# Optimization experiments

Measured on AMD Instinct MI355X. Metric: run time of the kernel, lower is better.

## Reference

```python
import jax, jax.numpy as jnp
import numpy as np

HIDDEN = 1024
NUM_EXPERTS = 64
MIN_K, MAX_K = 1, 4
THRESHOLD = 0.5
N_TOKENS = 32768


def setup_inputs() -> dict:
    key = jax.random.key(0)
    ks = jax.random.split(key, 6)
    std = 0.02
    h4 = HIDDEN // 4
    return {
        "hidden_states": jax.random.normal(ks[0], (N_TOKENS, HIDDEN), dtype=jnp.float32),
        "router_w": std * jax.random.normal(ks[1], (NUM_EXPERTS, HIDDEN), dtype=jnp.float32),
        "w1": std * jax.random.normal(ks[2], (h4, HIDDEN), dtype=jnp.float32),
        "b1": jnp.zeros((h4,), dtype=jnp.float32),
        "w2": std * jax.random.normal(ks[3], (1, h4), dtype=jnp.float32),
        "b2": jnp.zeros((1,), dtype=jnp.float32),
    }


def reference(hidden_states, router_w, w1, b1, w2, b2):
    # complexity predictor: Linear -> ReLU -> Linear -> Sigmoid, squeeze(-1)
    h = jax.nn.relu(hidden_states @ w1.T + b1)                     # [N, H/4]
    complexity = jax.nn.sigmoid(h @ w2.T + b2)[:, 0]               # [N]
    router_logits = hidden_states @ router_w.T                     # [N, E]

    adaptive_k = jnp.where(complexity > THRESHOLD, MAX_K, MIN_K)   # [N] int

    # vectorized adaptive top-k: take MAX_K everywhere, mask beyond k
    top_vals, top_idx = jax.lax.top_k(router_logits, MAX_K)        # [N, MAX_K]
    pos_mask = jnp.arange(MAX_K)[None, :] < adaptive_k[:, None]    # [N, MAX_K]
    masked_vals = jnp.where(pos_mask, top_vals, -jnp.inf)
    expert_weights = jax.nn.softmax(masked_vals, axis=-1)
    expert_weights = jnp.where(pos_mask, expert_weights, 0.0)      # zeros past k
    selected_experts = jnp.where(pos_mask, top_idx, 0)             # zeros past k

    # routing statistics
    probs = jax.nn.softmax(router_logits, axis=-1)                 # [N, E]
    expert_load = probs.mean(axis=0)                               # [E]
    load_variance = expert_load.var(ddof=1)                        # torch .var() is unbiased
    entropy = -(probs * jnp.log(probs + 1e-8)).sum(axis=-1).mean()

    return router_logits, selected_experts, expert_weights, load_variance, entropy
```

## Files before the change

### kernel.cpp

```cpp
#include <hip/hip_runtime.h>
#include <hip/hip_bf16.h>
#include <math.h>

#define NTOK 32768
#define HID  1024
#define NEXP 64
#define H4   256

typedef __attribute__((ext_vector_type(8))) short bf16x8;
typedef __attribute__((ext_vector_type(8))) unsigned short u16x8;
typedef __attribute__((ext_vector_type(4))) float f32x4;

static __device__ __forceinline__ ushort f2bf(float x) {
    unsigned u = __float_as_uint(x);
    unsigned r = (u + 0x7FFFu + ((u >> 16) & 1u)) >> 16;
    return (ushort)r;
}

static __device__ __forceinline__ void split3r(float x, ushort &h, ushort &m, ushort &l) {
    h = f2bf(x);
    const float r1 = x - __uint_as_float(((unsigned)h) << 16);
    m = f2bf(r1);
    const float r2 = r1 - __uint_as_float(((unsigned)m) << 16);
    l = f2bf(r2);
}

#define SWZ(row, us) ((us) ^ (((row) & 7) << 3))

__global__ __launch_bounds__(256) void prep_kernel(
    const float* __restrict__ W1, const float* __restrict__ RW,
    ushort* __restrict__ W1f, ushort* __restrict__ RWf)
{
    if (blockIdx.x < 256) {
        const int id = blockIdx.x * 256 + threadIdx.x;
        const int c  = id >> 8;
        const int k0 = (id & 255) * 4;
        const float4 v = *(const float4*)(W1 + (size_t)c * HID + k0);
        const int p = k0 >> 5, quad = (k0 >> 3) & 3, kk = k0 & 7;
        const int cg = c >> 6, j = (c >> 4) & 3, l15 = c & 15;
        const int lane = quad * 16 + l15;
        const size_t base = (size_t)p * 16384 + cg * 4096 + j * 1024 + lane * 8 + kk;
        const float xs[4] = {v.x, v.y, v.z, v.w};
        ushort hv[4], lv[4];
#pragma unroll
        for (int q = 0; q < 4; q++) {
            const ushort h = f2bf(xs[q]);
            hv[q] = h;
            lv[q] = f2bf(xs[q] - __uint_as_float(((unsigned)h) << 16));
        }
        *(ushort4*)(W1f + base)       = make_ushort4(hv[0], hv[1], hv[2], hv[3]);
        *(ushort4*)(W1f + base + 512) = make_ushort4(lv[0], lv[1], lv[2], lv[3]);
    } else {
        const int e  = blockIdx.x - 256;
        const int k0 = threadIdx.x * 4;
        const float4 v = *(const float4*)(RW + (size_t)e * HID + k0);
        const int p = k0 >> 5, quad = (k0 >> 3) & 3, kk = k0 & 7;
        const int cg = e >> 4, l15 = e & 15;
        const int lane = quad * 16 + l15;
        const size_t base = (size_t)p * 6144 + cg * 1536 + lane * 8 + kk;
        const float xs[4] = {v.x, v.y, v.z, v.w};
        ushort h[4], m[4], l[4];
#pragma unroll
        for (int q = 0; q < 4; q++) split3r(xs[q], h[q], m[q], l[q]);
        *(ushort4*)(RWf + base)        = make_ushort4(h[0], h[1], h[2], h[3]);
        *(ushort4*)(RWf + base + 512)  = make_ushort4(m[0], m[1], m[2], m[3]);
        *(ushort4*)(RWf + base + 1024) = make_ushort4(l[0], l[1], l[2], l[3]);
    }
}

template<int PH>
__device__ __forceinline__ void kstep(
    int p, int cg, int lane, int quad, int l15, int row, int kc,
    const float* __restrict__ xsrc,
    const ushort* __restrict__ RWf, const ushort* __restrict__ W1f,
    ushort (&Xh)[2][2048], ushort (&Xm)[2][2048], ushort (&Xl)[2][2048],
    bf16x8 (&rwh)[2], bf16x8 (&rwm)[2], bf16x8 (&rwl)[2],
    bf16x8 (&bwh)[2][4], bf16x8 (&bwl)[2][4],
    float4 (&xp)[2][2],
    f32x4 (&accL)[4], f32x4 (&accP)[4][4])
{
    {
        const ushort* __restrict__ rwp =
            RWf + (size_t)((p + 1) & 31) * 6144 + cg * 1536 + lane * 8;
        rwh[PH ^ 1] = *(const bf16x8*)(rwp);
        rwm[PH ^ 1] = *(const bf16x8*)(rwp + 512);
        rwl[PH ^ 1] = *(const bf16x8*)(rwp + 1024);
    }
    {
        const ushort* __restrict__ w1p =
            W1f + (size_t)((p + 1) & 31) * 16384 + cg * 4096 + lane * 8;
#pragma unroll
        for (int j = 0; j < 4; ++j) {
            bwh[PH ^ 1][j] = *(const bf16x8*)(w1p + j * 1024);
            bwl[PH ^ 1][j] = *(const bf16x8*)(w1p + j * 1024 + 512);
        }
    }
    xp[PH ^ 1][0] = *(const float4*)(xsrc + (size_t)((p + 2) & 31) * 32);
    xp[PH ^ 1][1] = *(const float4*)(xsrc + (size_t)((p + 2) & 31) * 32 + 4);

    bf16x8 axh[4], axm[4], axl[4];
#pragma unroll
    for (int f = 0; f < 4; ++f) {
        const int ra = f * 16 + l15;
        const int ua = SWZ(ra, ra * 32 + quad * 8);
        axh[f] = *(const bf16x8*)&Xh[PH][ua];
        axm[f] = *(const bf16x8*)&Xm[PH][ua];
        axl[f] = *(const bf16x8*)&Xl[PH][ua];
    }

    {
        const float xs[8] = {xp[PH][0].x, xp[PH][0].y, xp[PH][0].z, xp[PH][0].w,
                             xp[PH][1].x, xp[PH][1].y, xp[PH][1].z, xp[PH][1].w};
        u16x8 sh, sm, sl;
#pragma unroll
        for (int q = 0; q < 8; ++q) {
            ushort h, m, l;
            split3r(xs[q], h, m, l);
            sh[q] = h; sm[q] = m; sl[q] = l;
        }
        const int us = SWZ(row, row * 32 + kc * 8);
        *(u16x8*)&Xh[PH ^ 1][us] = sh;
        *(u16x8*)&Xm[PH ^ 1][us] = sm;
        *(u16x8*)&Xl[PH ^ 1][us] = sl;
    }

#pragma unroll
    for (int f = 0; f < 4; ++f) {
        accL[f] = __builtin_amdgcn_mfma_f32_16x16x32_bf16(axh[f], rwh[PH], accL[f], 0, 0, 0);
        accL[f] = __builtin_amdgcn_mfma_f32_16x16x32_bf16(axm[f], rwh[PH], accL[f], 0, 0, 0);
        accL[f] = __builtin_amdgcn_mfma_f32_16x16x32_bf16(axh[f], rwm[PH], accL[f], 0, 0, 0);
        accL[f] = __builtin_amdgcn_mfma_f32_16x16x32_bf16(axl[f], rwh[PH], accL[f], 0, 0, 0);
        accL[f] = __builtin_amdgcn_mfma_f32_16x16x32_bf16(axh[f], rwl[PH], accL[f], 0, 0, 0);
        accL[f] = __builtin_amdgcn_mfma_f32_16x16x32_bf16(axm[f], rwm[PH], accL[f], 0, 0, 0);
    }
#pragma unroll
    for (int j = 0; j < 4; ++j)
#pragma unroll
        for (int f = 0; f < 4; ++f) {
            accP[f][j] = __builtin_amdgcn_mfma_f32_16x16x32_bf16(axh[f], bwh[PH][j], accP[f][j], 0, 0, 0);
            accP[f][j] = __builtin_amdgcn_mfma_f32_16x16x32_bf16(axm[f], bwh[PH][j], accP[f][j], 0, 0, 0);
            accP[f][j] = __builtin_amdgcn_mfma_f32_16x16x32_bf16(axh[f], bwl[PH][j], accP[f][j], 0, 0, 0);
        }

    asm volatile("s_waitcnt lgkmcnt(0)" ::: "memory");
    __builtin_amdgcn_s_barrier();
    __builtin_amdgcn_sched_barrier(0);
}

__global__ __launch_bounds__(256, 2) void fused_mfma(
    const float* __restrict__ X,
    const ushort* __restrict__ RWf, const ushort* __restrict__ W1f,
    const float* __restrict__ B1, const float* __restrict__ W2,
    const float* __restrict__ B2,
    float* __restrict__ logits, float* __restrict__ sel,
    float* __restrict__ wts, float* __restrict__ load_sum,
    float* __restrict__ ent_sum)
{
    __shared__ __align__(16) ushort Xh[2][2048], Xm[2][2048], Xl[2][2048];
    __shared__ float red[4][64];
    __shared__ float Lt[64][65];

    const int tid  = threadIdx.x;
    const int lane = tid & 63;
    const int cg   = tid >> 6;
    const int quad = lane >> 4, l15 = lane & 15;
    const int tok0 = blockIdx.x * 64;

    const int row = tid >> 2;
    const int kc  = tid & 3;

    f32x4 accL[4];
    f32x4 accP[4][4];
#pragma unroll
    for (int f = 0; f < 4; f++) {
        accL[f] = (f32x4){0.f, 0.f, 0.f, 0.f};
#pragma unroll
        for (int j = 0; j < 4; j++) accP[f][j] = (f32x4){0.f, 0.f, 0.f, 0.f};
    }

    const float* __restrict__ xsrc = X + (size_t)(tok0 + row) * HID + kc * 8;

    bf16x8 rwh[2], rwm[2], rwl[2];
    bf16x8 bwh[2][4], bwl[2][4];
    float4 xp[2][2];

    {
        const float4 a0 = *(const float4*)(xsrc);
        const float4 a1 = *(const float4*)(xsrc + 4);
        const float xs[8] = {a0.x, a0.y, a0.z, a0.w, a1.x, a1.y, a1.z, a1.w};
        u16x8 sh, sm, sl;
#pragma unroll
        for (int q = 0; q < 8; ++q) {
            ushort h, m, l;
            split3r(xs[q], h, m, l);
            sh[q] = h; sm[q] = m; sl[q] = l;
        }
        const int us = SWZ(row, row * 32 + kc * 8);
        *(u16x8*)&Xh[0][us] = sh;
        *(u16x8*)&Xm[0][us] = sm;
        *(u16x8*)&Xl[0][us] = sl;
    }
    {
        const ushort* __restrict__ rwp = RWf + (size_t)cg * 1536 + lane * 8;
        rwh[0] = *(const bf16x8*)(rwp);
        rwm[0] = *(const bf16x8*)(rwp + 512);
        rwl[0] = *(const bf16x8*)(rwp + 1024);
        const ushort* __restrict__ w1p = W1f + (size_t)cg * 4096 + lane * 8;
#pragma unroll
        for (int j = 0; j < 4; ++j) {
            bwh[0][j] = *(const bf16x8*)(w1p + j * 1024);
            bwl[0][j] = *(const bf16x8*)(w1p + j * 1024 + 512);
        }
    }
    xp[0][0] = *(const float4*)(xsrc + 32);
    xp[0][1] = *(const float4*)(xsrc + 36);
    __syncthreads();

    for (int p = 0; p < 32; p += 2) {
        kstep<0>(p,     cg, lane, quad, l15, row, kc, xsrc, RWf, W1f,
                 Xh, Xm, Xl, rwh, rwm, rwl, bwh, bwl, xp, accL, accP);
        kstep<1>(p + 1, cg, lane, quad, l15, row, kc, xsrc, RWf, W1f,
                 Xh, Xm, Xl, rwh, rwm, rwl, bwh, bwl, xp, accL, accP);
    }

#pragma unroll
    for (int f = 0; f < 4; ++f)
#pragma unroll
        for (int r = 0; r < 4; ++r) {
            const int trow = f * 16 + quad * 4 + r;
            logits[(size_t)(tok0 + trow) * NEXP + cg * 16 + l15] = accL[f][r];
            Lt[trow][cg * 16 + l15] = accL[f][r];
        }

    float w2r[4], b1r[4];
#pragma unroll
    for (int j = 0; j < 4; ++j) {
        const int col = (cg * 4 + j) * 16 + l15;
        w2r[j] = W2[col];
        b1r[j] = B1[col];
    }
#pragma unroll
    for (int f = 0; f < 4; ++f) {
#pragma unroll
        for (int r = 0; r < 4; ++r) {
            float s = 0.f;
#pragma unroll
            for (int j = 0; j < 4; ++j) {
                const float hval = accP[f][j][r] + b1r[j];
                s = fmaf(w2r[j], fmaxf(hval, 0.f), s);
            }
            s += __shfl_xor(s, 1);
            s += __shfl_xor(s, 2);
            s += __shfl_xor(s, 4);
            s += __shfl_xor(s, 8);
            if (l15 == 0)
                red[cg][f * 16 + quad * 4 + r] = s;
        }
    }
    __syncthreads();

    if (cg == 0) {
        const int tok = tok0 + lane;

        float r[64];
#pragma unroll
        for (int e = 0; e < 64; e++) r[e] = Lt[lane][e];

        float v0 = -1e30f, v1 = -1e30f, v2 = -1e30f, v3 = -1e30f;
        int   i0 = 0, i1 = 0, i2 = 0, i3 = 0;
#pragma unroll
        for (int e = 0; e < 64; e++) {
            const float v = r[e];
            if (v > v3) {
                if (v > v2) {
                    if (v > v1) {
                        if (v > v0) { v3=v2;i3=i2; v2=v1;i2=i1; v1=v0;i1=i0; v0=v;i0=e; }
                        else        { v3=v2;i3=i2; v2=v1;i2=i1; v1=v;i1=e; }
                    } else          { v3=v2;i3=i2; v2=v;i2=e; }
                } else              { v3=v;i3=e; }
            }
        }

        const float s2 = red[0][lane] + red[1][lane] + red[2][lane]
                       + red[3][lane] + B2[0];
        const bool k4 = (s2 > 0.f);

        float w0, w1v, w2v, w3v;
        int   s1i, s2i, s3i;
        if (k4) {
            const float e0 = expf(v0 - v0), e1 = expf(v1 - v0);
            const float e2 = expf(v2 - v0), e3 = expf(v3 - v0);
            const float inv4 = 1.f / (e0 + e1 + e2 + e3);
            w0 = e0 * inv4; w1v = e1 * inv4; w2v = e2 * inv4; w3v = e3 * inv4;
            s1i = i1; s2i = i2; s3i = i3;
        } else {
            w0 = 1.f; w1v = 0.f; w2v = 0.f; w3v = 0.f;
            s1i = 0; s2i = 0; s3i = 0;
        }
        {
            float4 sv = {(float)i0, (float)s1i, (float)s2i, (float)s3i};
            float4 wv = {w0, w1v, w2v, w3v};
            *(float4*)(sel + (size_t)tok * 4) = sv;
            *(float4*)(wts + (size_t)tok * 4) = wv;
        }

        const float mx = v0;
        float S = 0.f, pz = 0.f;
#pragma unroll
        for (int e = 0; e < 64; e++) {
            const float z = r[e] - mx;
            const float t = expf(z);
            S += t; pz = fmaf(t, z, pz);
            r[e] = t;
        }
        const float inv = 1.f / S;
        float ent = logf(S) - pz * inv;

        float myload = 0.f;
#pragma unroll
        for (int e = 0; e < 64; e++) {
            float s = r[e] * inv;
            s += __shfl_xor(s, 1);
            s += __shfl_xor(s, 2);
            s += __shfl_xor(s, 4);
            s += __shfl_xor(s, 8);
            s += __shfl_xor(s, 16);
            s += __shfl_xor(s, 32);
            if (lane == e) myload = s;
        }
        atomicAdd(&load_sum[lane], myload);

        ent += __shfl_xor(ent, 1);
        ent += __shfl_xor(ent, 2);
        ent += __shfl_xor(ent, 4);
        ent += __shfl_xor(ent, 8);
        ent += __shfl_xor(ent, 16);
        ent += __shfl_xor(ent, 32);
        if (lane == 0) atomicAdd(ent_sum, ent);
    }
}

__global__ void finalize_kernel(const float* __restrict__ load_sum,
                                const float* __restrict__ ent_sum,
                                float* __restrict__ out_scal)
{
    const int lane = threadIdx.x;
    const float le = load_sum[lane] * (1.f / (float)NTOK);
    float s = le;
#pragma unroll
    for (int o = 32; o >= 1; o >>= 1) s += __shfl_xor(s, o);
    const float mean = s * (1.f / 64.f);
    const float d = le - mean;
    float v = d * d;
#pragma unroll
    for (int o = 32; o >= 1; o >>= 1) v += __shfl_xor(v, o);
    if (lane == 0) {
        out_scal[0] = v * (1.f / 63.f);
        out_scal[1] = ent_sum[0] * (1.f / (float)NTOK);
    }
}

extern "C" void kernel_launch(void* const* d_in, const int* in_sizes, int n_in,
                              void* d_out, int out_size, void* d_ws, size_t ws_size,
                              hipStream_t stream) {
    const float* X  = (const float*)d_in[0];
    const float* RW = (const float*)d_in[1];
    const float* W1 = (const float*)d_in[2];
    const float* B1 = (const float*)d_in[3];
    const float* W2 = (const float*)d_in[4];
    const float* B2 = (const float*)d_in[5];

    float* out    = (float*)d_out;
    float* logits = out;
    float* sel    = out + (size_t)NTOK * NEXP;
    float* wts    = sel + (size_t)NTOK * 4;
    float* scal   = wts + (size_t)NTOK * 4;

    float* s2ws     = (float*)d_ws;
    float* load_sum = s2ws + NTOK;
    float* ent_sum  = load_sum + 64;
    ushort* W1f = (ushort*)(s2ws + NTOK + 256);
    ushort* RWf = W1f + (size_t)32 * 16384;

    hipMemsetAsync(load_sum, 0, 65 * sizeof(float), stream);

    prep_kernel<<<320, 256, 0, stream>>>(W1, RW, W1f, RWf);
    fused_mfma<<<NTOK / 64, 256, 0, stream>>>(X, RWf, W1f, B1, W2, B2,
                                              logits, sel, wts, load_sum, ent_sum);
    finalize_kernel<<<1, 64, 0, stream>>>(load_sum, ent_sum, scal);
}
```

Baseline: 254.7 us.

## Switch to 32x32x16 MFMA tiles with 2x2 wave layout

Result: slower. 285.8 us (+12.2%).

```diff
diff --git a/kernel.cpp b/kernel.cpp
--- a/kernel.cpp
+++ b/kernel.cpp
@@ -7,9 +7,9 @@
 #define NEXP 64
 #define H4   256
 
-typedef __attribute__((ext_vector_type(8))) short bf16x8;
-typedef __attribute__((ext_vector_type(8))) unsigned short u16x8;
-typedef __attribute__((ext_vector_type(4))) float f32x4;
+typedef __attribute__((ext_vector_type(8)))  short bf16x8;
+typedef __attribute__((ext_vector_type(8)))  unsigned short u16x8;
+typedef __attribute__((ext_vector_type(16))) float f32x16;
 
 static __device__ __forceinline__ ushort f2bf(float x) {
     unsigned u = __float_as_uint(x);
@@ -36,10 +36,13 @@
         const int c  = id >> 8;
         const int k0 = (id & 255) * 4;
         const float4 v = *(const float4*)(W1 + (size_t)c * HID + k0);
-        const int p = k0 >> 5, quad = (k0 >> 3) & 3, kk = k0 & 7;
-        const int cg = c >> 6, j = (c >> 4) & 3, l15 = c & 15;
-        const int lane = quad * 16 + l15;
-        const size_t base = (size_t)p * 16384 + cg * 4096 + j * 1024 + lane * 8 + kk;
+        const int p  = k0 >> 5;
+        const int ks = (k0 >> 4) & 1;
+        const int h5 = (k0 >> 3) & 1;
+        const int i0 = k0 & 7;
+        const int tcj = c >> 5, c31 = c & 31;
+        const int lane = h5 * 32 + c31;
+        const size_t base = (size_t)p * 16384 + tcj * 2048 + ks * 1024 + lane * 8 + i0;
         const float xs[4] = {v.x, v.y, v.z, v.w};
         ushort hv[4], lv[4];
 #pragma unroll
@@ -54,10 +57,13 @@
         const int e  = blockIdx.x - 256;
         const int k0 = threadIdx.x * 4;
         const float4 v = *(const float4*)(RW + (size_t)e * HID + k0);
-        const int p = k0 >> 5, quad = (k0 >> 3) & 3, kk = k0 & 7;
-        const int cg = e >> 4, l15 = e & 15;
-        const int lane = quad * 16 + l15;
-        const size_t base = (size_t)p * 6144 + cg * 1536 + lane * 8 + kk;
+        const int p  = k0 >> 5;
+        const int ks = (k0 >> 4) & 1;
+        const int h5 = (k0 >> 3) & 1;
+        const int i0 = k0 & 7;
+        const int tc = e >> 5, c31 = e & 31;
+        const int lane = h5 * 32 + c31;
+        const size_t base = (size_t)p * 6144 + tc * 3072 + ks * 1536 + lane * 8 + i0;
         const float xs[4] = {v.x, v.y, v.z, v.w};
         ushort h[4], m[4], l[4];
 #pragma unroll
@@ -70,42 +76,42 @@
 
 template<int PH>
 __device__ __forceinline__ void kstep(
-    int p, int cg, int lane, int quad, int l15, int row, int kc,
+    int p, int tr, int tc, int lane, int l31, int h5, int row, int kc,
     const float* __restrict__ xsrc,
     const ushort* __restrict__ RWf, const ushort* __restrict__ W1f,
     ushort (&Xh)[2][2048], ushort (&Xm)[2][2048], ushort (&Xl)[2][2048],
-    bf16x8 (&rwh)[2], bf16x8 (&rwm)[2], bf16x8 (&rwl)[2],
-    bf16x8 (&bwh)[2][4], bf16x8 (&bwl)[2][4],
     float4 (&xp)[2][2],
-    f32x4 (&accL)[4], f32x4 (&accP)[4][4])
+    f32x16 &accL, f32x16 (&accP)[4])
 {
-    {
-        const ushort* __restrict__ rwp =
-            RWf + (size_t)((p + 1) & 31) * 6144 + cg * 1536 + lane * 8;
-        rwh[PH ^ 1] = *(const bf16x8*)(rwp);
-        rwm[PH ^ 1] = *(const bf16x8*)(rwp + 512);
-        rwl[PH ^ 1] = *(const bf16x8*)(rwp + 1024);
-    }
-    {
-        const ushort* __restrict__ w1p =
-            W1f + (size_t)((p + 1) & 31) * 16384 + cg * 4096 + lane * 8;
+    const ushort* __restrict__ rwp = RWf + (size_t)p * 6144 + tc * 3072 + lane * 8;
+    bf16x8 rwh[2], rwm[2], rwl[2];
+#pragma unroll
+    for (int ks = 0; ks < 2; ++ks) {
+        rwh[ks] = *(const bf16x8*)(rwp + ks * 1536);
+        rwm[ks] = *(const bf16x8*)(rwp + ks * 1536 + 512);
+        rwl[ks] = *(const bf16x8*)(rwp + ks * 1536 + 1024);
+    }
+    const ushort* __restrict__ w1p = W1f + (size_t)p * 16384 + (tc * 4) * 2048 + lane * 8;
+    bf16x8 bwh[2][4], bwl[2][4];
+#pragma unroll
+    for (int ks = 0; ks < 2; ++ks)
 #pragma unroll
         for (int j = 0; j < 4; ++j) {
-            bwh[PH ^ 1][j] = *(const bf16x8*)(w1p + j * 1024);
-            bwl[PH ^ 1][j] = *(const bf16x8*)(w1p + j * 1024 + 512);
-        }
-    }
+            bwh[ks][j] = *(const bf16x8*)(w1p + j * 2048 + ks * 1024);
+            bwl[ks][j] = *(const bf16x8*)(w1p + j * 2048 + ks * 1024 + 512);
+        }
+
     xp[PH ^ 1][0] = *(const float4*)(xsrc + (size_t)((p + 2) & 31) * 32);
     xp[PH ^ 1][1] = *(const float4*)(xsrc + (size_t)((p + 2) & 31) * 32 + 4);
 
-    bf16x8 axh[4], axm[4], axl[4];
-#pragma unroll
-    for (int f = 0; f < 4; ++f) {
-        const int ra = f * 16 + l15;
-        const int ua = SWZ(ra, ra * 32 + quad * 8);
-        axh[f] = *(const bf16x8*)&Xh[PH][ua];
-        axm[f] = *(const bf16x8*)&Xm[PH][ua];
-        axl[f] = *(const bf16x8*)&Xl[PH][ua];
+    const int arow = tr * 32 + l31;
+    bf16x8 axh[2], axm[2], axl[2];
+#pragma unroll
+    for (int ks = 0; ks < 2; ++ks) {
+        const int ua = SWZ(arow, arow * 32 + ks * 16 + h5 * 8);
+        axh[ks] = *(const bf16x8*)&Xh[PH][ua];
+        axm[ks] = *(const bf16x8*)&Xm[PH][ua];
+        axl[ks] = *(const bf16x8*)&Xl[PH][ua];
     }
 
     {
@@ -125,22 +131,20 @@
     }
 
 #pragma unroll
-    for (int f = 0; f < 4; ++f) {
-        accL[f] = __builtin_amdgcn_mfma_f32_16x16x32_bf16(axh[f], rwh[PH], accL[f], 0, 0, 0);
-        accL[f] = __builtin_amdgcn_mfma_f32_16x16x32_bf16(axm[f], rwh[PH], accL[f], 0, 0, 0);
-        accL[f] = __builtin_amdgcn_mfma_f32_16x16x32_bf16(axh[f], rwm[PH], accL[f], 0, 0, 0);
-        accL[f] = __builtin_amdgcn_mfma_f32_16x16x32_bf16(axl[f], rwh[PH], accL[f], 0, 0, 0);
-        accL[f] = __builtin_amdgcn_mfma_f32_16x16x32_bf16(axh[f], rwl[PH], accL[f], 0, 0, 0);
-        accL[f] = __builtin_amdgcn_mfma_f32_16x16x32_bf16(axm[f], rwm[PH], accL[f], 0, 0, 0);
-    }
-#pragma unroll
-    for (int j = 0; j < 4; ++j)
-#pragma unroll
-        for (int f = 0; f < 4; ++f) {
-            accP[f][j] = __builtin_amdgcn_mfma_f32_16x16x32_bf16(axh[f], bwh[PH][j], accP[f][j], 0, 0, 0);
-            accP[f][j] = __builtin_amdgcn_mfma_f32_16x16x32_bf16(axm[f], bwh[PH][j], accP[f][j], 0, 0, 0);
-            accP[f][j] = __builtin_amdgcn_mfma_f32_16x16x32_bf16(axh[f], bwl[PH][j], accP[f][j], 0, 0, 0);
-        }
+    for (int ks = 0; ks < 2; ++ks) {
+        accL = __builtin_amdgcn_mfma_f32_32x32x16_bf16(axh[ks], rwh[ks], accL, 0, 0, 0);
+        accL = __builtin_amdgcn_mfma_f32_32x32x16_bf16(axm[ks], rwh[ks], accL, 0, 0, 0);
+        accL = __builtin_amdgcn_mfma_f32_32x32x16_bf16(axh[ks], rwm[ks], accL, 0, 0, 0);
+        accL = __builtin_amdgcn_mfma_f32_32x32x16_bf16(axl[ks], rwh[ks], accL, 0, 0, 0);
+        accL = __builtin_amdgcn_mfma_f32_32x32x16_bf16(axh[ks], rwl[ks], accL, 0, 0, 0);
+        accL = __builtin_amdgcn_mfma_f32_32x32x16_bf16(axm[ks], rwm[ks], accL, 0, 0, 0);
+#pragma unroll
+        for (int j = 0; j < 4; ++j) {
+            accP[j] = __builtin_amdgcn_mfma_f32_32x32x16_bf16(axh[ks], bwh[ks][j], accP[j], 0, 0, 0);
+            accP[j] = __builtin_amdgcn_mfma_f32_32x32x16_bf16(axm[ks], bwh[ks][j], accP[j], 0, 0, 0);
+            accP[j] = __builtin_amdgcn_mfma_f32_32x32x16_bf16(axh[ks], bwl[ks][j], accP[j], 0, 0, 0);
+        }
+    }
 
     asm volatile("s_waitcnt lgkmcnt(0)" ::: "memory");
     __builtin_amdgcn_s_barrier();
@@ -157,31 +161,32 @@
     float* __restrict__ ent_sum)
 {
     __shared__ __align__(16) ushort Xh[2][2048], Xm[2][2048], Xl[2][2048];
-    __shared__ float red[4][64];
+    __shared__ float red[2][64];
     __shared__ float Lt[64][65];
 
     const int tid  = threadIdx.x;
     const int lane = tid & 63;
-    const int cg   = tid >> 6;
-    const int quad = lane >> 4, l15 = lane & 15;
+    const int w    = tid >> 6;
+    const int tr   = w >> 1;
+    const int tc   = w & 1;
+    const int l31  = lane & 31;
+    const int h5   = lane >> 5;
     const int tok0 = blockIdx.x * 64;
 
     const int row = tid >> 2;
     const int kc  = tid & 3;
 
-    f32x4 accL[4];
-    f32x4 accP[4][4];
-#pragma unroll
-    for (int f = 0; f < 4; f++) {
-        accL[f] = (f32x4){0.f, 0.f, 0.f, 0.f};
-#pragma unroll
-        for (int j = 0; j < 4; j++) accP[f][j] = (f32x4){0.f, 0.f, 0.f, 0.f};
-    }
+    f32x16 accL;
+    f32x16 accP[4];
+#pragma unroll
+    for (int i = 0; i < 16; i++) accL[i] = 0.f;
+#pragma unroll
+    for (int j = 0; j < 4; j++)
+#pragma unroll
+        for (int i = 0; i < 16; i++) accP[j][i] = 0.f;
 
     const float* __restrict__ xsrc = X + (size_t)(tok0 + row) * HID + kc * 8;
 
-    bf16x8 rwh[2], rwm[2], rwl[2];
-    bf16x8 bwh[2][4], bwl[2][4];
     float4 xp[2][2];
 
     {
@@ -200,66 +205,51 @@
         *(u16x8*)&Xm[0][us] = sm;
         *(u16x8*)&Xl[0][us] = sl;
     }
-    {
-        const ushort* __restrict__ rwp = RWf + (size_t)cg * 1536 + lane * 8;
-        rwh[0] = *(const bf16x8*)(rwp);
-        rwm[0] = *(const bf16x8*)(rwp + 512);
-        rwl[0] = *(const bf16x8*)(rwp + 1024);
-        const ushort* __restrict__ w1p = W1f + (size_t)cg * 4096 + lane * 8;
-#pragma unroll
-        for (int j = 0; j < 4; ++j) {
-            bwh[0][j] = *(const bf16x8*)(w1p + j * 1024);
-            bwl[0][j] = *(const bf16x8*)(w1p + j * 1024 + 512);
-        }
-    }
     xp[0][0] = *(const float4*)(xsrc + 32);
     xp[0][1] = *(const float4*)(xsrc + 36);
     __syncthreads();
 
     for (int p = 0; p < 32; p += 2) {
-        kstep<0>(p,     cg, lane, quad, l15, row, kc, xsrc, RWf, W1f,
-                 Xh, Xm, Xl, rwh, rwm, rwl, bwh, bwl, xp, accL, accP);
-        kstep<1>(p + 1, cg, lane, quad, l15, row, kc, xsrc, RWf, W1f,
-                 Xh, Xm, Xl, rwh, rwm, rwl, bwh, bwl, xp, accL, accP);
-    }
-
-#pragma unroll
-    for (int f = 0; f < 4; ++f)
-#pragma unroll
-        for (int r = 0; r < 4; ++r) {
-            const int trow = f * 16 + quad * 4 + r;
-            logits[(size_t)(tok0 + trow) * NEXP + cg * 16 + l15] = accL[f][r];
-            Lt[trow][cg * 16 + l15] = accL[f][r];
-        }
+        kstep<0>(p,     tr, tc, lane, l31, h5, row, kc, xsrc, RWf, W1f,
+                 Xh, Xm, Xl, xp, accL, accP);
+        kstep<1>(p + 1, tr, tc, lane, l31, h5, row, kc, xsrc, RWf, W1f,
+                 Xh, Xm, Xl, xp, accL, accP);
+    }
+
+#pragma unroll
+    for (int r = 0; r < 16; ++r) {
+        const int orow = (r & 3) + 8 * (r >> 2) + 4 * h5;
+        const int trow = tr * 32 + orow;
+        logits[(size_t)(tok0 + trow) * NEXP + tc * 32 + l31] = accL[r];
+        Lt[trow][tc * 32 + l31] = accL[r];
+    }
 
     float w2r[4], b1r[4];
 #pragma unroll
     for (int j = 0; j < 4; ++j) {
-        const int col = (cg * 4 + j) * 16 + l15;
+        const int col = (tc * 4 + j) * 32 + l31;
         w2r[j] = W2[col];
         b1r[j] = B1[col];
     }
 #pragma unroll
-    for (int f = 0; f < 4; ++f) {
-#pragma unroll
-        for (int r = 0; r < 4; ++r) {
-            float s = 0.f;
-#pragma unroll
-            for (int j = 0; j < 4; ++j) {
-                const float hval = accP[f][j][r] + b1r[j];
-                s = fmaf(w2r[j], fmaxf(hval, 0.f), s);
-            }
-            s += __shfl_xor(s, 1);
-            s += __shfl_xor(s, 2);
-            s += __shfl_xor(s, 4);
-            s += __shfl_xor(s, 8);
-            if (l15 == 0)
-                red[cg][f * 16 + quad * 4 + r] = s;
-        }
+    for (int r = 0; r < 16; ++r) {
+        float s = 0.f;
+#pragma unroll
+        for (int j = 0; j < 4; ++j) {
+            const float hval = accP[j][r] + b1r[j];
+            s = fmaf(w2r[j], fmaxf(hval, 0.f), s);
+        }
+        s += __shfl_xor(s, 1);
+        s += __shfl_xor(s, 2);
+        s += __shfl_xor(s, 4);
+        s += __shfl_xor(s, 8);
+        s += __shfl_xor(s, 16);
+        if (l31 == 0)
+            red[tc][tr * 32 + (r & 3) + 8 * (r >> 2) + 4 * h5] = s;
     }
     __syncthreads();
 
-    if (cg == 0) {
+    if (w == 0) {
         const int tok = tok0 + lane;
 
         float r[64];
@@ -281,8 +271,7 @@
             }
         }
 
-        const float s2 = red[0][lane] + red[1][lane] + red[2][lane]
-                       + red[3][lane] + B2[0];
+        const float s2 = red[0][lane] + red[1][lane] + B2[0];
         const bool k4 = (s2 > 0.f);
 
         float w0, w1v, w2v, w3v;
```

## Load X fragments directly from global into registers, dropping LDS staging and barriers

Applied to the files above, without the earlier changes.

After: 327.5 us. 28.6% more time.

```diff
diff --git a/kernel.cpp b/kernel.cpp
--- a/kernel.cpp
+++ b/kernel.cpp
@@ -8,7 +8,6 @@
 #define H4   256
 
 typedef __attribute__((ext_vector_type(8))) short bf16x8;
-typedef __attribute__((ext_vector_type(8))) unsigned short u16x8;
 typedef __attribute__((ext_vector_type(4))) float f32x4;
 
 static __device__ __forceinline__ ushort f2bf(float x) {
@@ -24,8 +23,6 @@
     const float r2 = r1 - __uint_as_float(((unsigned)m) << 16);
     l = f2bf(r2);
 }
-
-#define SWZ(row, us) ((us) ^ (((row) & 7) << 3))
 
 __global__ __launch_bounds__(256) void prep_kernel(
     const float* __restrict__ W1, const float* __restrict__ RW,
@@ -70,15 +67,20 @@
 
 template<int PH>
 __device__ __forceinline__ void kstep(
-    int p, int cg, int lane, int quad, int l15, int row, int kc,
-    const float* __restrict__ xsrc,
+    int p, int cg, int lane, int quad, int l15,
+    const float* __restrict__ xrow0,
     const ushort* __restrict__ RWf, const ushort* __restrict__ W1f,
-    ushort (&Xh)[2][2048], ushort (&Xm)[2][2048], ushort (&Xl)[2][2048],
     bf16x8 (&rwh)[2], bf16x8 (&rwm)[2], bf16x8 (&rwl)[2],
-    bf16x8 (&bwh)[2][4], bf16x8 (&bwl)[2][4],
-    float4 (&xp)[2][2],
+    float4 (&xa)[2][4][2],
     f32x4 (&accL)[4], f32x4 (&accP)[4][4])
 {
+    const ushort* __restrict__ w1p = W1f + (size_t)p * 16384 + cg * 4096 + lane * 8;
+    bf16x8 bwh[4], bwl[4];
+#pragma unroll
+    for (int j = 0; j < 4; ++j) {
+        bwh[j] = *(const bf16x8*)(w1p + j * 1024);
+        bwl[j] = *(const bf16x8*)(w1p + j * 1024 + 512);
+    }
     {
         const ushort* __restrict__ rwp =
             RWf + (size_t)((p + 1) & 31) * 6144 + cg * 1536 + lane * 8;
@@ -87,64 +89,39 @@
         rwl[PH ^ 1] = *(const bf16x8*)(rwp + 1024);
     }
     {
-        const ushort* __restrict__ w1p =
-            W1f + (size_t)((p + 1) & 31) * 16384 + cg * 4096 + lane * 8;
+        const int kn = ((p + 1) & 31) * 32 + quad * 8;
+#pragma unroll
+        for (int f = 0; f < 4; ++f) {
+            const float* __restrict__ src = xrow0 + (size_t)(f * 16 + l15) * HID + kn;
+            xa[PH ^ 1][f][0] = *(const float4*)(src);
+            xa[PH ^ 1][f][1] = *(const float4*)(src + 4);
+        }
+    }
+
+#pragma unroll
+    for (int f = 0; f < 4; ++f) {
+        const float4 a0 = xa[PH][f][0], a1 = xa[PH][f][1];
+        const float xs[8] = {a0.x, a0.y, a0.z, a0.w, a1.x, a1.y, a1.z, a1.w};
+        ushort hv[8], mv[8], lv[8];
+#pragma unroll
+        for (int q = 0; q < 8; ++q) split3r(xs[q], hv[q], mv[q], lv[q]);
+        bf16x8 axh, axm, axl;
+#pragma unroll
+        for (int q = 0; q < 8; ++q) { axh[q] = (short)hv[q]; axm[q] = (short)mv[q]; axl[q] = (short)lv[q]; }
+
+        accL[f] = __builtin_amdgcn_mfma_f32_16x16x32_bf16(axh, rwh[PH], accL[f], 0, 0, 0);
+        accL[f] = __builtin_amdgcn_mfma_f32_16x16x32_bf16(axm, rwh[PH], accL[f], 0, 0, 0);
+        accL[f] = __builtin_amdgcn_mfma_f32_16x16x32_bf16(axh, rwm[PH], accL[f], 0, 0, 0);
+        accL[f] = __builtin_amdgcn_mfma_f32_16x16x32_bf16(axl, rwh[PH], accL[f], 0, 0, 0);
+        accL[f] = __builtin_amdgcn_mfma_f32_16x16x32_bf16(axh, rwl[PH], accL[f], 0, 0, 0);
+        accL[f] = __builtin_amdgcn_mfma_f32_16x16x32_bf16(axm, rwm[PH], accL[f], 0, 0, 0);
 #pragma unroll
         for (int j = 0; j < 4; ++j) {
-            bwh[PH ^ 1][j] = *(const bf16x8*)(w1p + j * 1024);
-            bwl[PH ^ 1][j] = *(const bf16x8*)(w1p + j * 1024 + 512);
-        }
-    }
-    xp[PH ^ 1][0] = *(const float4*)(xsrc + (size_t)((p + 2) & 31) * 32);
-    xp[PH ^ 1][1] = *(const float4*)(xsrc + (size_t)((p + 2) & 31) * 32 + 4);
-
-    bf16x8 axh[4], axm[4], axl[4];
-#pragma unroll
-    for (int f = 0; f < 4; ++f) {
-        const int ra = f * 16 + l15;
-        const int ua = SWZ(ra, ra * 32 + quad * 8);
-        axh[f] = *(const bf16x8*)&Xh[PH][ua];
-        axm[f] = *(const bf16x8*)&Xm[PH][ua];
-        axl[f] = *(const bf16x8*)&Xl[PH][ua];
-    }
-
-    {
-        const float xs[8] = {xp[PH][0].x, xp[PH][0].y, xp[PH][0].z, xp[PH][0].w,
-                             xp[PH][1].x, xp[PH][1].y, xp[PH][1].z, xp[PH][1].w};
-        u16x8 sh, sm, sl;
-#pragma unroll
-        for (int q = 0; q < 8; ++q) {
-            ushort h, m, l;
-            split3r(xs[q], h, m, l);
-            sh[q] = h; sm[q] = m; sl[q] = l;
-        }
-        const int us = SWZ(row, row * 32 + kc * 8);
-        *(u16x8*)&Xh[PH ^ 1][us] = sh;
-        *(u16x8*)&Xm[PH ^ 1][us] = sm;
-        *(u16x8*)&Xl[PH ^ 1][us] = sl;
-    }
-
-#pragma unroll
-    for (int f = 0; f < 4; ++f) {
-        accL[f] = __builtin_amdgcn_mfma_f32_16x16x32_bf16(axh[f], rwh[PH], accL[f], 0, 0, 0);
-        accL[f] = __builtin_amdgcn_mfma_f32_16x16x32_bf16(axm[f], rwh[PH], accL[f], 0, 0, 0);
-        accL[f] = __builtin_amdgcn_mfma_f32_16x16x32_bf16(axh[f], rwm[PH], accL[f], 0, 0, 0);
-        accL[f] = __builtin_amdgcn_mfma_f32_16x16x32_bf16(axl[f], rwh[PH], accL[f], 0, 0, 0);
-        accL[f] = __builtin_amdgcn_mfma_f32_16x16x32_bf16(axh[f], rwl[PH], accL[f], 0, 0, 0);
-        accL[f] = __builtin_amdgcn_mfma_f32_16x16x32_bf16(axm[f], rwm[PH], accL[f], 0, 0, 0);
-    }
-#pragma unroll
-    for (int j = 0; j < 4; ++j)
-#pragma unroll
-        for (int f = 0; f < 4; ++f) {
-            accP[f][j] = __builtin_amdgcn_mfma_f32_16x16x32_bf16(axh[f], bwh[PH][j], accP[f][j], 0, 0, 0);
-            accP[f][j] = __builtin_amdgcn_mfma_f32_16x16x32_bf16(axm[f], bwh[PH][j], accP[f][j], 0, 0, 0);
-            accP[f][j] = __builtin_amdgcn_mfma_f32_16x16x32_bf16(axh[f], bwl[PH][j], accP[f][j], 0, 0, 0);
-        }
-
-    asm volatile("s_waitcnt lgkmcnt(0)" ::: "memory");
-    __builtin_amdgcn_s_barrier();
-    __builtin_amdgcn_sched_barrier(0);
+            accP[f][j] = __builtin_amdgcn_mfma_f32_16x16x32_bf16(axh, bwh[j], accP[f][j], 0, 0, 0);
+            accP[f][j] = __builtin_amdgcn_mfma_f32_16x16x32_bf16(axm, bwh[j], accP[f][j], 0, 0, 0);
+            accP[f][j] = __builtin_amdgcn_mfma_f32_16x16x32_bf16(axh, bwl[j], accP[f][j], 0, 0, 0);
+        }
+    }
 }
 
 __global__ __launch_bounds__(256, 2) void fused_mfma(
@@ -156,7 +133,6 @@
     float* __restrict__ wts, float* __restrict__ load_sum,
     float* __restrict__ ent_sum)
 {
-    __shared__ __align__(16) ushort Xh[2][2048], Xm[2][2048], Xl[2][2048];
     __shared__ float red[4][64];
     __shared__ float Lt[64][65];
 
@@ -166,9 +142,6 @@
     const int quad = lane >> 4, l15 = lane & 15;
     const int tok0 = blockIdx.x * 64;
 
-    const int row = tid >> 2;
-    const int kc  = tid & 3;
-
     f32x4 accL[4];
     f32x4 accP[4][4];
 #pragma unroll
@@ -178,49 +151,29 @@
         for (int j = 0; j < 4; j++) accP[f][j] = (f32x4){0.f, 0.f, 0.f, 0.f};
     }
 
-    const float* __restrict__ xsrc = X + (size_t)(tok0 + row) * HID + kc * 8;
+    const float* __restrict__ xrow0 = X + (size_t)tok0 * HID;
 
     bf16x8 rwh[2], rwm[2], rwl[2];
-    bf16x8 bwh[2][4], bwl[2][4];
-    float4 xp[2][2];
-
-    {
-        const float4 a0 = *(const float4*)(xsrc);
-        const float4 a1 = *(const float4*)(xsrc + 4);
-        const float xs[8] = {a0.x, a0.y, a0.z, a0.w, a1.x, a1.y, a1.z, a1.w};
-        u16x8 sh, sm, sl;
-#pragma unroll
-        for (int q = 0; q < 8; ++q) {
-            ushort h, m, l;
-            split3r(xs[q], h, m, l);
-            sh[q] = h; sm[q] = m; sl[q] = l;
-        }
-        const int us = SWZ(row, row * 32 + kc * 8);
-        *(u16x8*)&Xh[0][us] = sh;
-        *(u16x8*)&Xm[0][us] = sm;
-        *(u16x8*)&Xl[0][us] = sl;
+    float4 xa[2][4][2];
+
+#pragma unroll
+    for (int f = 0; f < 4; ++f) {
+        const float* __restrict__ src = xrow0 + (size_t)(f * 16 + l15) * HID + quad * 8;
+        xa[0][f][0] = *(const float4*)(src);
+        xa[0][f][1] = *(const float4*)(src + 4);
     }
     {
         const ushort* __restrict__ rwp = RWf + (size_t)cg * 1536 + lane * 8;
         rwh[0] = *(const bf16x8*)(rwp);
         rwm[0] = *(const bf16x8*)(rwp + 512);
         rwl[0] = *(const bf16x8*)(rwp + 1024);
-        const ushort* __restrict__ w1p = W1f + (size_t)cg * 4096 + lane * 8;
-#pragma unroll
-        for (int j = 0; j < 4; ++j) {
-            bwh[0][j] = *(const bf16x8*)(w1p + j * 1024);
-            bwl[0][j] = *(const bf16x8*)(w1p + j * 1024 + 512);
-        }
-    }
-    xp[0][0] = *(const float4*)(xsrc + 32);
-    xp[0][1] = *(const float4*)(xsrc + 36);
-    __syncthreads();
+    }
 
     for (int p = 0; p < 32; p += 2) {
-        kstep<0>(p,     cg, lane, quad, l15, row, kc, xsrc, RWf, W1f,
-                 Xh, Xm, Xl, rwh, rwm, rwl, bwh, bwl, xp, accL, accP);
-        kstep<1>(p + 1, cg, lane, quad, l15, row, kc, xsrc, RWf, W1f,
-                 Xh, Xm, Xl, rwh, rwm, rwl, bwh, bwl, xp, accL, accP);
+        kstep<0>(p,     cg, lane, quad, l15, xrow0, RWf, W1f,
+                 rwh, rwm, rwl, xa, accL, accP);
+        kstep<1>(p + 1, cg, lane, quad, l15, xrow0, RWf, W1f,
+                 rwh, rwm, rwl, xa, accL, accP);
     }
 
 #pragma unroll
```
